# Optimization experiments

Measured on AMD Instinct MI355X. Metric: run time of the kernel, lower is better.

The kernel has to match this reference:

```python
import jax, jax.numpy as jnp
import numpy as np

B, L, D = 8, 2048, 64


def setup_inputs() -> dict:
    key = jax.random.key(0)
    kq, kk, kv = jax.random.split(key, 3)
    query = jax.random.normal(kq, (B, L, D), dtype=jnp.float32)
    key_t = jax.random.normal(kk, (B, L, D), dtype=jnp.float32)
    value = jax.random.normal(kv, (B, L, D), dtype=jnp.float32)
    return {"query": query, "key": key_t, "value": value}


def reference(query, key, value):
    d = query.shape[-1]
    # e = Q K^T / sqrt(d_k)   -> [B, Lq, Lk]
    scale = 1.0 / np.sqrt(float(d)).astype(np.float32)
    e = jnp.einsum("bqd,bkd->bqk", query, key) * scale
    # stable softmax over keys (matches exp(e - max)/sum in source)
    attention = jax.nn.softmax(e, axis=-1)
    # v = A V   -> [B, Lq, Dv]
    return jnp.einsum("bqk,bkd->bqd", attention, value)
```

## Files before the change

### kernel.cpp

```cpp
#include <hip/hip_runtime.h>


#define B_ 8
#define L_ 2048
#define D_ 64
#define NT 256

typedef _Float16 half8_t __attribute__((ext_vector_type(8)));
typedef _Float16 half4_t __attribute__((ext_vector_type(4)));
typedef float f32x4 __attribute__((ext_vector_type(4)));

#define SCALE_LOG2E 0.1803368801111244f

__global__ __launch_bounds__(NT) void prepass_frag(
    const float* __restrict__ K, const float* __restrict__ V,
    _Float16* __restrict__ K16F, _Float16* __restrict__ VT16F)
{
    const int blk = blockIdx.x;
    const int t = threadIdx.x;
    if (blk < 512) {
        const int b  = blk & 7;
        const int kt = blk >> 3;
        const int p    = t >> 6;
        const int lane = t & 63;
        const int quad = lane >> 4;
        const int l15  = lane & 15;
        const int s = p >> 1, c = p & 1;
        const int row = kt * 32 + s * 16 + l15;
        const float* kp = K + ((size_t)b * L_ + row) * D_ + c * 32 + quad * 8;
        const float4 f0 = *(const float4*)kp;
        const float4 f1 = *(const float4*)(kp + 4);
        half8_t w;
        w[0] = (_Float16)f0.x; w[1] = (_Float16)f0.y;
        w[2] = (_Float16)f0.z; w[3] = (_Float16)f0.w;
        w[4] = (_Float16)f1.x; w[5] = (_Float16)f1.y;
        w[6] = (_Float16)f1.z; w[7] = (_Float16)f1.w;
        *(half8_t*)&K16F[((size_t)(b * 64 + kt) * 4 + p) * 512 + lane * 8] = w;
    } else {
        const int vb = blk - 512;
        const int b  = vb & 7;
        const int kt = vb >> 3;
        #pragma unroll
        for (int i = 0; i < 2; ++i) {
            const int slot = i * NT + t;
            const int p    = slot >> 6;
            const int lane = slot & 63;
            const int quad = lane >> 4;
            const int l15  = lane & 15;
            const int d = p >> 1, ks = p & 1;
            const int row = kt * 32 + ks * 16 + quad * 4;
            const int col = d * 16 + l15;
            const float* vp = V + ((size_t)b * L_ + row) * D_ + col;
            half4_t a;
            a[0] = (_Float16)vp[0];
            a[1] = (_Float16)vp[D_];
            a[2] = (_Float16)vp[2 * D_];
            a[3] = (_Float16)vp[3 * D_];
            *(half4_t*)&VT16F[((size_t)(b * 64 + kt) * 8 + p) * 256 + lane * 4] = a;
        }
    }
}


#define LOADK(KT, BK)                                                           \
    {                                                                           \
        const int ktc_ = (KT) & 63;                                             \
        _Pragma("unroll") for (int s = 0; s < 2; ++s)                           \
        _Pragma("unroll") for (int c = 0; c < 2; ++c)                           \
            BK[s][c] = *(const half8_t*)&KbF[((size_t)ktc_ * 4 + s * 2 + c) * 512 + lane * 8]; \
    }

#define LOADV(KT, AV)                                                           \
    {                                                                           \
        const int ktc_ = (KT) & 63;                                             \
        _Pragma("unroll") for (int d = 0; d < 4; ++d)                           \
        _Pragma("unroll") for (int ks = 0; ks < 2; ++ks)                        \
            AV[d][ks] = *(const half4_t*)&VbF[((size_t)ktc_ * 8 + d * 2 + ks) * 256 + lane * 4]; \
    }

#define PROC(BK, AV)                                                            \
    {                                                                           \
        half4_t pb[2][4];                                                       \
        _Pragma("unroll") for (int ks = 0; ks < 2; ++ks)                        \
        _Pragma("unroll") for (int qf = 0; qf < 4; ++qf) {                      \
            f32x4 acc = (f32x4){0.f, 0.f, 0.f, 0.f};                            \
            acc = __builtin_amdgcn_mfma_f32_16x16x32_f16(BK[ks][0], bq[qf][0], acc, 0, 0, 0); \
            acc = __builtin_amdgcn_mfma_f32_16x16x32_f16(BK[ks][1], bq[qf][1], acc, 0, 0, 0); \
            const float p0 = __builtin_exp2f(acc[0]);                           \
            const float p1 = __builtin_exp2f(acc[1]);                           \
            const float p2 = __builtin_exp2f(acc[2]);                           \
            const float p3 = __builtin_exp2f(acc[3]);                           \
            lacc[qf] += (p0 + p1) + (p2 + p3);                                  \
            half4_t pv;                                                         \
            pv[0] = (_Float16)p0; pv[1] = (_Float16)p1;                         \
            pv[2] = (_Float16)p2; pv[3] = (_Float16)p3;                         \
            pb[ks][qf] = pv;                                                    \
        }                                                                       \
        _Pragma("unroll") for (int qf = 0; qf < 4; ++qf)                        \
        _Pragma("unroll") for (int d = 0; d < 4; ++d)                           \
        _Pragma("unroll") for (int ks = 0; ks < 2; ++ks)                        \
            ofr[qf][d] = __builtin_amdgcn_mfma_f32_16x16x16f16(AV[d][ks], pb[ks][qf], ofr[qf][d], 0, 0, 0); \
    }

__global__ __launch_bounds__(512, 2) void attn_q64(
    const float* __restrict__ Q,
    const _Float16* __restrict__ K16F,
    const _Float16* __restrict__ VT16F,
    float* __restrict__ O)
{
    __shared__ float Ored[512 * 17];
    __shared__ float Lred[512];

    const int t    = threadIdx.x;
    const int wave = t >> 6;
    const int lane = t & 63;
    const int quad = lane >> 4;
    const int l15  = lane & 15;

    const int b   = blockIdx.x & 7;
    const int qbi = blockIdx.x >> 3;
    const int qb  = qbi * 64;
    const int kt0 = wave * 8;

    const _Float16* KbF = K16F + (size_t)b * 64 * 4 * 512;
    const _Float16* VbF = VT16F + (size_t)b * 64 * 8 * 256;

    half8_t bq[4][2];
    #pragma unroll
    for (int qf = 0; qf < 4; ++qf) {
        const float* qp = Q + ((size_t)b * L_ + qb + qf * 16 + l15) * D_ + quad * 8;
        #pragma unroll
        for (int c = 0; c < 2; ++c) {
            const float4 f0 = *(const float4*)(qp + c * 32);
            const float4 f1 = *(const float4*)(qp + c * 32 + 4);
            bq[qf][c][0] = (_Float16)(f0.x * SCALE_LOG2E);
            bq[qf][c][1] = (_Float16)(f0.y * SCALE_LOG2E);
            bq[qf][c][2] = (_Float16)(f0.z * SCALE_LOG2E);
            bq[qf][c][3] = (_Float16)(f0.w * SCALE_LOG2E);
            bq[qf][c][4] = (_Float16)(f1.x * SCALE_LOG2E);
            bq[qf][c][5] = (_Float16)(f1.y * SCALE_LOG2E);
            bq[qf][c][6] = (_Float16)(f1.z * SCALE_LOG2E);
            bq[qf][c][7] = (_Float16)(f1.w * SCALE_LOG2E);
        }
    }

    f32x4 ofr[4][4];
    #pragma unroll
    for (int qf = 0; qf < 4; ++qf)
        #pragma unroll
        for (int d = 0; d < 4; ++d)
            ofr[qf][d] = (f32x4){0.f, 0.f, 0.f, 0.f};
    float lacc[4] = {0.f, 0.f, 0.f, 0.f};

    half8_t bkA[2][2], bkB[2][2];
    half4_t avA[4][2], avB[4][2];
    LOADK(kt0, bkA);
    LOADV(kt0, avA);
    for (int it = 0; it < 4; ++it) {
        const int kta = kt0 + it * 2;
        LOADK(kta + 1, bkB);
        LOADV(kta + 1, avB);
        PROC(bkA, avA);
        LOADK(kta + 2, bkA);
        LOADV(kta + 2, avA);
        PROC(bkB, avB);
    }

    #pragma unroll
    for (int qf = 0; qf < 4; ++qf) {
        float v = lacc[qf];
        v += __shfl_xor(v, 16, 64);
        v += __shfl_xor(v, 32, 64);
        lacc[qf] = v;
    }
    if (quad == 0) {
        #pragma unroll
        for (int qf = 0; qf < 4; ++qf)
            Lred[wave * 64 + qf * 16 + l15] = lacc[qf];
    }

    #pragma unroll
    for (int qf = 0; qf < 4; ++qf) {
        __syncthreads();
        float* dst = &Ored[(wave * 64 + lane) * 17];
        #pragma unroll
        for (int d = 0; d < 4; ++d)
            #pragma unroll
            for (int r = 0; r < 4; ++r)
                dst[d * 4 + r] = ofr[qf][d][r];
        __syncthreads();
        if (wave < 4) {
            float lt = 0.f;
            #pragma unroll
            for (int w2 = 0; w2 < 8; ++w2)
                lt += Lred[w2 * 64 + qf * 16 + l15];
            const float inv = 1.0f / lt;
            f32x4 osum = (f32x4){0.f, 0.f, 0.f, 0.f};
            #pragma unroll
            for (int w2 = 0; w2 < 8; ++w2) {
                const float* src = &Ored[(w2 * 64 + lane) * 17 + wave * 4];
                osum[0] += src[0]; osum[1] += src[1];
                osum[2] += src[2]; osum[3] += src[3];
            }
            float4 outv;
            outv.x = osum[0] * inv; outv.y = osum[1] * inv;
            outv.z = osum[2] * inv; outv.w = osum[3] * inv;
            *(float4*)&O[((size_t)b * L_ + qb + qf * 16 + l15) * D_ + wave * 16 + quad * 4] = outv;
        }
    }
}

#define KS 72
__global__ __launch_bounds__(NT) void attn_mfma_f16(
    const float* __restrict__ Q, const float* __restrict__ K,
    const float* __restrict__ V, float* __restrict__ O)
{
    __shared__ __align__(16) _Float16 Kt[64 * KS];
    __shared__ __align__(16) _Float16 Vt[D_ * KS];
    __shared__ __align__(16) _Float16 Pt[4][16 * KS];

    const int t = threadIdx.x;
    const int wave = t >> 6, lane = t & 63, quad = lane >> 4, l15 = lane & 15;
    const int bpb = L_ / 64;
    const int b = blockIdx.x / bpb;
    const int qb = (blockIdx.x % bpb) * 64 + wave * 16;
    const size_t boff = (size_t)b * L_ * D_;

    half8_t aq[2];
    {
        const float* qp = Q + boff + (size_t)(qb + l15) * D_ + quad * 8;
        #pragma unroll
        for (int c = 0; c < 2; ++c) {
            const float4* p4 = (const float4*)(qp + c * 32);
            const float4 f0 = p4[0], f1 = p4[1];
            aq[c][0] = (_Float16)f0.x; aq[c][1] = (_Float16)f0.y;
            aq[c][2] = (_Float16)f0.z; aq[c][3] = (_Float16)f0.w;
            aq[c][4] = (_Float16)f1.x; aq[c][5] = (_Float16)f1.y;
            aq[c][6] = (_Float16)f1.z; aq[c][7] = (_Float16)f1.w;
        }
    }
    f32x4 ofr[4];
    #pragma unroll
    for (int d = 0; d < 4; ++d) ofr[d] = (f32x4){0.f, 0.f, 0.f, 0.f};
    float lacc[4] = {0.f, 0.f, 0.f, 0.f};
    const int skey = t & 63, sdg = t >> 6;
    _Float16* Pw = &Pt[wave][0];

    for (int kt = 0; kt < L_ / 64; ++kt) {
        __syncthreads();
        {
            const float4* kg4 = (const float4*)(K + boff + (size_t)(kt * 64 + skey) * D_ + sdg * 16);
            const float4 f0 = kg4[0], f1 = kg4[1], f2 = kg4[2], f3 = kg4[3];
            half8_t w0, w1;
            w0[0] = (_Float16)f0.x; w0[1] = (_Float16)f0.y;
            w0[2] = (_Float16)f0.z; w0[3] = (_Float16)f0.w;
            w0[4] = (_Float16)f1.x; w0[5] = (_Float16)f1.y;
            w0[6] = (_Float16)f1.z; w0[7] = (_Float16)f1.w;
            w1[0] = (_Float16)f2.x; w1[1] = (_Float16)f2.y;
            w1[2] = (_Float16)f2.z; w1[3] = (_Float16)f2.w;
            w1[4] = (_Float16)f3.x; w1[5] = (_Float16)f3.y;
            w1[6] = (_Float16)f3.z; w1[7] = (_Float16)f3.w;
            *(half8_t*)&Kt[skey * KS + sdg * 16] = w0;
            *(half8_t*)&Kt[skey * KS + sdg * 16 + 8] = w1;
        }
        {
            const float4* vg4 = (const float4*)(V + boff + (size_t)(kt * 64 + skey) * D_ + sdg * 16);
            #pragma unroll
            for (int i = 0; i < 4; ++i) {
                const float4 f = vg4[i];
                const int d0 = sdg * 16 + i * 4;
                Vt[(d0 + 0) * KS + skey] = (_Float16)f.x;
                Vt[(d0 + 1) * KS + skey] = (_Float16)f.y;
                Vt[(d0 + 2) * KS + skey] = (_Float16)f.z;
                Vt[(d0 + 3) * KS + skey] = (_Float16)f.w;
            }
        }
        __syncthreads();
        #pragma unroll
        for (int s = 0; s < 4; ++s) {
            const half8_t bk0 = *(const half8_t*)&Kt[(s * 16 + l15) * KS + quad * 8];
            const half8_t bk1 = *(const half8_t*)&Kt[(s * 16 + l15) * KS + 32 + quad * 8];
            f32x4 sc = (f32x4){0.f, 0.f, 0.f, 0.f};
            sc = __builtin_amdgcn_mfma_f32_16x16x32_f16(aq[0], bk0, sc, 0, 0, 0);
            sc = __builtin_amdgcn_mfma_f32_16x16x32_f16(aq[1], bk1, sc, 0, 0, 0);
            #pragma unroll
            for (int r = 0; r < 4; ++r) {
                const float p = __expf(sc[r] * 0.125f);
                lacc[r] += p;
                Pw[(quad * 4 + r) * KS + s * 16 + l15] = (_Float16)p;
            }
        }
        __syncthreads();
        #pragma unroll
        for (int c = 0; c < 2; ++c) {
            const half8_t ap = *(const half8_t*)&Pw[l15 * KS + c * 32 + quad * 8];
            #pragma unroll
            for (int d = 0; d < 4; ++d) {
                const half8_t bv = *(const half8_t*)&Vt[(d * 16 + l15) * KS + c * 32 + quad * 8];
                ofr[d] = __builtin_amdgcn_mfma_f32_16x16x32_f16(ap, bv, ofr[d], 0, 0, 0);
            }
        }
    }
    #pragma unroll
    for (int r = 0; r < 4; ++r) {
        float v = lacc[r];
        v += __shfl_xor(v, 1, 64);
        v += __shfl_xor(v, 2, 64);
        v += __shfl_xor(v, 4, 64);
        v += __shfl_xor(v, 8, 64);
        lacc[r] = v;
    }
    #pragma unroll
    for (int r = 0; r < 4; ++r) {
        const float inv = 1.0f / lacc[r];
        float* orow = O + boff + (size_t)(qb + quad * 4 + r) * D_ + l15;
        #pragma unroll
        for (int d = 0; d < 4; ++d) orow[d * 16] = ofr[d][r] * inv;
    }
}

extern "C" void kernel_launch(void* const* d_in, const int* in_sizes, int n_in,
                              void* d_out, int out_size, void* d_ws, size_t ws_size,
                              hipStream_t stream) {
    const float* Q = (const float*)d_in[0];
    const float* K = (const float*)d_in[1];
    const float* V = (const float*)d_in[2];
    float* O = (float*)d_out;

    if (ws_size >= (size_t)8 * 1024 * 1024) {
        _Float16* K16F  = (_Float16*)d_ws;
        _Float16* VT16F = K16F + (size_t)1048576;
        prepass_frag<<<1024, NT, 0, stream>>>(K, V, K16F, VT16F);
        attn_q64<<<256, 512, 0, stream>>>(Q, K16F, VT16F, O);
    } else {
        attn_mfma_f16<<<256, NT, 0, stream>>>(Q, K, V, O);
    }
}
```

Baseline: 87.27 us.

## Split attention work across 16 waves by key group and output-dim half

```diff
diff --git a/kernel.cpp b/kernel.cpp
--- a/kernel.cpp
+++ b/kernel.cpp
@@ -56,7 +56,7 @@
             a[1] = (_Float16)vp[D_];
             a[2] = (_Float16)vp[2 * D_];
             a[3] = (_Float16)vp[3 * D_];
-            *(half4_t*)&VT16F[((size_t)(b * 64 + kt) * 8 + p) * 256 + lane * 4] = a;
+            *(half4_t*)&VT16F[((size_t)(b * 64 + kt) * 4 + d) * 512 + lane * 8 + ks * 4] = a;
         }
     }
 }
@@ -73,16 +73,16 @@
 #define LOADV(KT, AV)                                                           \
     {                                                                           \
         const int ktc_ = (KT) & 63;                                             \
-        _Pragma("unroll") for (int d = 0; d < 4; ++d)                           \
+        _Pragma("unroll") for (int j = 0; j < 2; ++j)                           \
+            AV[j] = *(const half8_t*)&VbF[((size_t)ktc_ * 4 + dh * 2 + j) * 512 + lane * 8]; \
+    }
+
+#define PROC(BK, AV)                                                            \
+    _Pragma("unroll") for (int qp = 0; qp < 2; ++qp) {                          \
+        half4_t pb[2][2];                                                       \
         _Pragma("unroll") for (int ks = 0; ks < 2; ++ks)                        \
-            AV[d][ks] = *(const half4_t*)&VbF[((size_t)ktc_ * 8 + d * 2 + ks) * 256 + lane * 4]; \
-    }
-
-#define PROC(BK, AV)                                                            \
-    {                                                                           \
-        half4_t pb[2][4];                                                       \
-        _Pragma("unroll") for (int ks = 0; ks < 2; ++ks)                        \
-        _Pragma("unroll") for (int qf = 0; qf < 4; ++qf) {                      \
+        _Pragma("unroll") for (int q2 = 0; q2 < 2; ++q2) {                      \
+            const int qf = qp * 2 + q2;                                         \
             f32x4 acc = (f32x4){0.f, 0.f, 0.f, 0.f};                            \
             acc = __builtin_amdgcn_mfma_f32_16x16x32_f16(BK[ks][0], bq[qf][0], acc, 0, 0, 0); \
             acc = __builtin_amdgcn_mfma_f32_16x16x32_f16(BK[ks][1], bq[qf][1], acc, 0, 0, 0); \
@@ -94,41 +94,55 @@
             half4_t pv;                                                         \
             pv[0] = (_Float16)p0; pv[1] = (_Float16)p1;                         \
             pv[2] = (_Float16)p2; pv[3] = (_Float16)p3;                         \
-            pb[ks][qf] = pv;                                                    \
+            pb[ks][q2] = pv;                                                    \
         }                                                                       \
-        _Pragma("unroll") for (int qf = 0; qf < 4; ++qf)                        \
-        _Pragma("unroll") for (int d = 0; d < 4; ++d)                           \
-        _Pragma("unroll") for (int ks = 0; ks < 2; ++ks)                        \
-            ofr[qf][d] = __builtin_amdgcn_mfma_f32_16x16x16f16(AV[d][ks], pb[ks][qf], ofr[qf][d], 0, 0, 0); \
-    }
-
-__global__ __launch_bounds__(512, 2) void attn_q64(
+        _Pragma("unroll") for (int j = 0; j < 2; ++j) {                         \
+            const half4_t alo = __builtin_shufflevector(AV[j], AV[j], 0, 1, 2, 3); \
+            const half4_t ahi = __builtin_shufflevector(AV[j], AV[j], 4, 5, 6, 7); \
+            _Pragma("unroll") for (int q2 = 0; q2 < 2; ++q2) {                  \
+                const int qf = qp * 2 + q2;                                     \
+                ofr[qf][j] = __builtin_amdgcn_mfma_f32_16x16x16f16(alo, pb[0][q2], ofr[qf][j], 0, 0, 0); \
+                ofr[qf][j] = __builtin_amdgcn_mfma_f32_16x16x16f16(ahi, pb[1][q2], ofr[qf][j], 0, 0, 0); \
+            }                                                                   \
+        }                                                                       \
+    }
+
+__global__ __launch_bounds__(1024) void attn_dsplit(
     const float* __restrict__ Q,
     const _Float16* __restrict__ K16F,
     const _Float16* __restrict__ VT16F,
     float* __restrict__ O)
 {
-    __shared__ float Ored[512 * 17];
-    __shared__ float Lred[512];
+    __shared__ __align__(16) float SH[9728];
 
     const int t    = threadIdx.x;
     const int wave = t >> 6;
     const int lane = t & 63;
     const int quad = lane >> 4;
     const int l15  = lane & 15;
+    const int kg   = wave >> 1;
+    const int dh   = wave & 1;
 
     const int b   = blockIdx.x & 7;
     const int qbi = blockIdx.x >> 3;
     const int qb  = qbi * 64;
-    const int kt0 = wave * 8;
+    const int kt0 = kg * 8;
 
     const _Float16* KbF = K16F + (size_t)b * 64 * 4 * 512;
-    const _Float16* VbF = VT16F + (size_t)b * 64 * 8 * 256;
+    const _Float16* VbF = VT16F + (size_t)b * 64 * 4 * 512;
+
+    {
+        const int qr = t >> 4;
+        const int c4 = t & 15;
+        const float4 qv = *(const float4*)&Q[((size_t)b * L_ + qb + qr) * D_ + c4 * 4];
+        *(float4*)&SH[qr * 68 + c4 * 4] = qv;
+    }
+    __syncthreads();
 
     half8_t bq[4][2];
     #pragma unroll
     for (int qf = 0; qf < 4; ++qf) {
-        const float* qp = Q + ((size_t)b * L_ + qb + qf * 16 + l15) * D_ + quad * 8;
+        const float* qp = &SH[(qf * 16 + l15) * 68 + quad * 8];
         #pragma unroll
         for (int c = 0; c < 2; ++c) {
             const float4 f0 = *(const float4*)(qp + c * 32);
@@ -144,68 +158,72 @@
         }
     }
 
-    f32x4 ofr[4][4];
+    f32x4 ofr[4][2];
     #pragma unroll
     for (int qf = 0; qf < 4; ++qf)
         #pragma unroll
-        for (int d = 0; d < 4; ++d)
-            ofr[qf][d] = (f32x4){0.f, 0.f, 0.f, 0.f};
+        for (int j = 0; j < 2; ++j)
+            ofr[qf][j] = (f32x4){0.f, 0.f, 0.f, 0.f};
     float lacc[4] = {0.f, 0.f, 0.f, 0.f};
 
-    half8_t bkA[2][2], bkB[2][2];
-    half4_t avA[4][2], avB[4][2];
+    half8_t bkA[2][2], bkB[2][2], av[2];
     LOADK(kt0, bkA);
-    LOADV(kt0, avA);
     for (int it = 0; it < 4; ++it) {
         const int kta = kt0 + it * 2;
         LOADK(kta + 1, bkB);
-        LOADV(kta + 1, avB);
-        PROC(bkA, avA);
+        LOADV(kta, av);
+        PROC(bkA, av);
         LOADK(kta + 2, bkA);
-        LOADV(kta + 2, avA);
-        PROC(bkB, avB);
-    }
-
+        LOADV(kta + 1, av);
+        PROC(bkB, av);
+    }
+
+    float lsum[4];
     #pragma unroll
     for (int qf = 0; qf < 4; ++qf) {
         float v = lacc[qf];
         v += __shfl_xor(v, 16, 64);
         v += __shfl_xor(v, 32, 64);
-        lacc[qf] = v;
-    }
-    if (quad == 0) {
+        lsum[qf] = v;
+    }
+    float* Ored = &SH[0];
+    float* Lred = &SH[9216];
+    if (quad == 0 && dh == 0) {
         #pragma unroll
         for (int qf = 0; qf < 4; ++qf)
-            Lred[wave * 64 + qf * 16 + l15] = lacc[qf];
+            Lred[kg * 64 + qf * 16 + l15] = lsum[qf];
     }
 
     #pragma unroll
     for (int qf = 0; qf < 4; ++qf) {
         __syncthreads();
-        float* dst = &Ored[(wave * 64 + lane) * 17];
-        #pragma unroll
-        for (int d = 0; d < 4; ++d)
+        float* dst = &Ored[(wave * 64 + lane) * 9];
+        #pragma unroll
+        for (int j = 0; j < 2; ++j)
             #pragma unroll
             for (int r = 0; r < 4; ++r)
-                dst[d * 4 + r] = ofr[qf][d][r];
+                dst[j * 4 + r] = ofr[qf][j][r];
         __syncthreads();
         if (wave < 4) {
+            const int dhr = wave & 1;
+            const int dr  = wave >> 1;
             float lt = 0.f;
             #pragma unroll
-            for (int w2 = 0; w2 < 8; ++w2)
-                lt += Lred[w2 * 64 + qf * 16 + l15];
+            for (int k2 = 0; k2 < 8; ++k2)
+                lt += Lred[k2 * 64 + qf * 16 + l15];
             const float inv = 1.0f / lt;
             f32x4 osum = (f32x4){0.f, 0.f, 0.f, 0.f};
             #pragma unroll
-            for (int w2 = 0; w2 < 8; ++w2) {
-                const float* src = &Ored[(w2 * 64 + lane) * 17 + wave * 4];
+            for (int k2 = 0; k2 < 8; ++k2) {
+                const float* src = &Ored[((k2 * 2 + dhr) * 64 + lane) * 9 + dr * 4];
                 osum[0] += src[0]; osum[1] += src[1];
                 osum[2] += src[2]; osum[3] += src[3];
             }
             float4 outv;
             outv.x = osum[0] * inv; outv.y = osum[1] * inv;
             outv.z = osum[2] * inv; outv.w = osum[3] * inv;
-            *(float4*)&O[((size_t)b * L_ + qb + qf * 16 + l15) * D_ + wave * 16 + quad * 4] = outv;
+            *(float4*)&O[((size_t)b * L_ + qb + qf * 16 + l15) * D_
+                         + dhr * 32 + dr * 16 + quad * 4] = outv;
         }
     }
 }
@@ -331,7 +349,7 @@
         _Float16* K16F  = (_Float16*)d_ws;
         _Float16* VT16F = K16F + (size_t)1048576;
         prepass_frag<<<1024, NT, 0, stream>>>(K, V, K16F, VT16F);
-        attn_q64<<<256, 512, 0, stream>>>(Q, K16F, VT16F, O);
+        attn_dsplit<<<256, 1024, 0, stream>>>(Q, K16F, VT16F, O);
     } else {
         attn_mfma_f16<<<256, NT, 0, stream>>>(Q, K, V, O);
     }
```

New measurement: 145.7 us. +66.9%, slower.
